# Kernel tuning notes

Measured on AMD Instinct MI355X. Metric: run time of the kernel, lower is better.

Reference implementation:

```python
import jax, jax.numpy as jnp
import numpy as np

D_MODEL = 1024
NUM_HEADS = 16
D_K = D_MODEL // NUM_HEADS


def setup_inputs() -> dict:
    key = jax.random.key(0)
    ks = jax.random.split(key, 11)
    B, S = 2, 2048
    s = 1.0 / np.sqrt(D_MODEL)
    return {
        "query": jax.random.normal(ks[0], (B, S, D_MODEL), jnp.float32),
        "key": jax.random.normal(ks[1], (B, S, D_MODEL), jnp.float32),
        "value": jax.random.normal(ks[2], (B, S, D_MODEL), jnp.float32),
        "Wq": jax.random.normal(ks[3], (D_MODEL, D_MODEL), jnp.float32) * s,
        "bq": jnp.zeros((D_MODEL,), jnp.float32),
        "Wk": jax.random.normal(ks[4], (D_MODEL, D_MODEL), jnp.float32) * s,
        "bk": jnp.zeros((D_MODEL,), jnp.float32),
        "Wv": jax.random.normal(ks[5], (D_MODEL, D_MODEL), jnp.float32) * s,
        "bv": jnp.zeros((D_MODEL,), jnp.float32),
        "Wo": jax.random.normal(ks[6], (D_MODEL, D_MODEL), jnp.float32) * s,
        "bo": jnp.zeros((D_MODEL,), jnp.float32),
    }


def _split_heads(x):
    # [B, S, D] -> [B, H, S, d_k]
    B, S, _ = x.shape
    return x.reshape(B, S, NUM_HEADS, D_K).transpose(0, 2, 1, 3)


def reference(query, key, value, Wq, bq, Wk, bk, Wv, bv, Wo, bo):
    B, S, _ = query.shape
    q = _split_heads(query @ Wq + bq)   # [B, H, S, d_k]
    k = _split_heads(key @ Wk + bk)
    v = _split_heads(value @ Wv + bv)
    scores = jnp.einsum("bhqd,bhkd->bhqk", q, k) / jnp.sqrt(jnp.float32(D_K))
    attention_weights = jax.nn.softmax(scores, axis=-1)  # [B, H, S, S]
    context = jnp.einsum("bhqk,bhkd->bhqd", attention_weights, v)
    context = context.transpose(0, 2, 1, 3).reshape(B, S, D_MODEL)
    output = context @ Wo + bo
    return (output, attention_weights)
```

## Files before the change

### kernel.cpp

```cpp
#include <hip/hip_runtime.h>
#include <hip/hip_bf16.h>


#define SEQ   2048
#define DMODEL 1024
#define NH    16
#define DKH   64

typedef __attribute__((ext_vector_type(8))) short  short8;
typedef __attribute__((ext_vector_type(4))) float  floatx4;

__device__ __forceinline__ short f2bf(float f) {
    __hip_bfloat16 h = __float2bfloat16(f);
    return *reinterpret_cast<short*>(&h);
}

__device__ __forceinline__ void gload_lds16(const short* g, short* l) {
    __builtin_amdgcn_global_load_lds(
        (const __attribute__((address_space(1))) void*)g,
        (__attribute__((address_space(3))) void*)l, 16, 0, 0);
}

__global__ void conv_f32_bf16(const float* __restrict__ src, short* __restrict__ dst, int n4) {
    int i = blockIdx.x * blockDim.x + threadIdx.x;
    if (i < n4) {
        float4 v = reinterpret_cast<const float4*>(src)[i];
        short4 o;
        o.x = f2bf(v.x); o.y = f2bf(v.y); o.z = f2bf(v.z); o.w = f2bf(v.w);
        reinterpret_cast<short4*>(dst)[i] = o;
    }
}

__global__ void conv_wt(const float* __restrict__ W, short* __restrict__ Wt) {
    __shared__ short T[64 * 72];
    int tid = threadIdx.x;
    int bk = blockIdx.y, bn = blockIdx.x;
    for (int i = 0; i < 4; i++) {
        int ch = i * 256 + tid;
        int r = ch >> 4, c4 = (ch & 15) * 4;
        float4 v = *(const float4*)&W[(size_t)(bk * 64 + r) * 1024 + bn * 64 + c4];
        T[(c4 + 0) * 72 + r] = f2bf(v.x);
        T[(c4 + 1) * 72 + r] = f2bf(v.y);
        T[(c4 + 2) * 72 + r] = f2bf(v.z);
        T[(c4 + 3) * 72 + r] = f2bf(v.w);
    }
    __syncthreads();
    for (int i = 0; i < 2; i++) {
        int ch = i * 256 + tid;
        int n = ch >> 3, k8 = (ch & 7) * 8;
        *(short8*)&Wt[(size_t)(bn * 64 + n) * 1024 + bk * 64 + k8] = *(const short8*)&T[n * 72 + k8];
    }
}

__global__ __launch_bounds__(256, 3) void gemm_bf16(
    const short* __restrict__ A, const short* __restrict__ Bt,
    const float* __restrict__ bias, void* __restrict__ dst, int mode)
{
    __shared__ __align__(16) short As[128 * 32];
    __shared__ __align__(16) short Bs[64 * 32];
    int tid = threadIdx.x;
    int wave = tid >> 6, lane = tid & 63, quad = lane >> 4, l15 = lane & 15;
    int bm = blockIdx.y, bn = blockIdx.x;

    floatx4 acc[2][4];
    for (int i = 0; i < 2; i++) for (int j = 0; j < 4; j++) acc[i][j] = (floatx4){0.f, 0.f, 0.f, 0.f};

    for (int kb = 0; kb < 32; kb++) {
        for (int r = 0; r < 2; r++) {
            int ch = r * 256 + tid;
            int row = ch >> 2, kq = (ch & 3) * 8;
            gload_lds16(&A[(size_t)(bm * 128 + row) * 1024 + kb * 32 + kq],
                        &As[(r * 256 + wave * 64) * 8]);
        }
        {
            int row = tid >> 2, kq = (tid & 3) * 8;
            gload_lds16(&Bt[(size_t)(bn * 64 + row) * 1024 + kb * 32 + kq],
                        &Bs[(wave * 64) * 8]);
        }
        __syncthreads();
        short8 ar[2], br[4];
        for (int mt = 0; mt < 2; mt++) ar[mt] = *(const short8*)&As[(wave * 32 + mt * 16 + l15) * 32 + quad * 8];
        for (int nt = 0; nt < 4; nt++) br[nt] = *(const short8*)&Bs[(nt * 16 + l15) * 32 + quad * 8];
        for (int mt = 0; mt < 2; mt++)
            for (int nt = 0; nt < 4; nt++)
                acc[mt][nt] = __builtin_amdgcn_mfma_f32_16x16x32_bf16(ar[mt], br[nt], acc[mt][nt], 0, 0, 0);
        __syncthreads();
    }

    for (int mt = 0; mt < 2; mt++) {
        for (int nt = 0; nt < 4; nt++) {
            int col = bn * 64 + nt * 16 + l15;
            float bb = bias[col];
            for (int r = 0; r < 4; r++) {
                int row = bm * 128 + wave * 32 + mt * 16 + quad * 4 + r;
                float v = acc[mt][nt][r] + bb;
                if (mode == 3) {
                    ((float*)dst)[(size_t)row * 1024 + col] = v;
                } else {
                    int b = row >> 11, s = row & 2047, h = col >> 6, dk = col & 63;
                    size_t idx;
                    if (mode == 0) idx = ((size_t)(b * NH + h) * SEQ + s) * DKH + dk;
                    else           idx = ((size_t)(b * NH + h) * DKH + dk) * SEQ + s;
                    ((short*)dst)[idx] = f2bf(v);
                }
            }
        }
    }
}

__global__ __launch_bounds__(256, 2) void attn(
    const short* __restrict__ Q,
    const short* __restrict__ K,
    const short* __restrict__ Vt,
    float* __restrict__ wout,
    short* __restrict__ ctx)
{
    __shared__ __align__(16) short Qs [64 * 72];
    __shared__ __align__(16) short Ks [128 * 72];
    __shared__ __align__(16) short Vts[64 * 136];
    __shared__ __align__(16) short Ps [64 * 136];
    __shared__ float partial[4][64];
    __shared__ float rinv[64];

    int tid = threadIdx.x, wave = tid >> 6, lane = tid & 63, quad = lane >> 4, l15 = lane & 15;
    int qt = blockIdx.x, bh = blockIdx.y;
    int b = bh >> 4, h = bh & 15;
    const short* qb  = Q  + ((size_t)bh * SEQ + qt * 64) * DKH;
    const short* kbp = K  + (size_t)bh * SEQ * DKH;
    const short* vtb = Vt + (size_t)bh * DKH * SEQ;

    for (int c = 0; c < 2; c++) {
        int ch = tid * 2 + c; int row = ch >> 3, d = (ch & 7) * 8;
        *(short8*)&Qs[row * 72 + d] = *(const short8*)&qb[row * 64 + d];
    }

    float rs[4][4];
    for (int i = 0; i < 4; i++) for (int r = 0; r < 4; r++) rs[i][r] = 0.f;
    floatx4 cacc[4];
    for (int i = 0; i < 4; i++) cacc[i] = (floatx4){0.f, 0.f, 0.f, 0.f};
    int nbase = wave * 32;

    for (int kb = 0; kb < SEQ / 128; kb++) {
        __syncthreads();
        for (int c = 0; c < 4; c++) {
            int ch = tid * 4 + c; int row = ch >> 3, d = (ch & 7) * 8;
            *(short8*)&Ks[row * 72 + d] = *(const short8*)&kbp[(size_t)(kb * 128 + row) * 64 + d];
        }
        for (int c = 0; c < 4; c++) {
            int ch = tid * 4 + c; int dd = ch >> 4, kq = (ch & 15) * 8;
            *(short8*)&Vts[dd * 136 + kq] = *(const short8*)&vtb[(size_t)dd * SEQ + kb * 128 + kq];
        }
        __syncthreads();

        floatx4 sacc[4][2];
        for (int mt = 0; mt < 4; mt++) for (int nt = 0; nt < 2; nt++) sacc[mt][nt] = (floatx4){0.f, 0.f, 0.f, 0.f};
        for (int kt = 0; kt < 2; kt++) {
            short8 ar[4], br[2];
            for (int mt = 0; mt < 4; mt++) ar[mt] = *(const short8*)&Qs[(mt * 16 + l15) * 72 + kt * 32 + quad * 8];
            for (int nt = 0; nt < 2; nt++) br[nt] = *(const short8*)&Ks[(nbase + nt * 16 + l15) * 72 + kt * 32 + quad * 8];
            for (int mt = 0; mt < 4; mt++)
                for (int nt = 0; nt < 2; nt++)
                    sacc[mt][nt] = __builtin_amdgcn_mfma_f32_16x16x32_bf16(ar[mt], br[nt], sacc[mt][nt], 0, 0, 0);
        }
        for (int mt = 0; mt < 4; mt++) {
            for (int r = 0; r < 4; r++) {
                float e0 = __expf(sacc[mt][0][r] * 0.125f);
                float e1 = __expf(sacc[mt][1][r] * 0.125f);
                int row = mt * 16 + quad * 4 + r;
                Ps[row * 136 + nbase + l15]      = f2bf(e0);
                Ps[row * 136 + nbase + 16 + l15] = f2bf(e1);
                rs[mt][r] += e0 + e1;
            }
        }
        __syncthreads();
        for (int kt = 0; kt < 4; kt++) {
            short8 pa = *(const short8*)&Ps[(wave * 16 + l15) * 136 + kt * 32 + quad * 8];
            for (int nt = 0; nt < 4; nt++) {
                short8 vb = *(const short8*)&Vts[(nt * 16 + l15) * 136 + kt * 32 + quad * 8];
                cacc[nt] = __builtin_amdgcn_mfma_f32_16x16x32_bf16(pa, vb, cacc[nt], 0, 0, 0);
            }
        }
    }

    for (int mt = 0; mt < 4; mt++) {
        for (int r = 0; r < 4; r++) {
            float s = rs[mt][r];
            s += __shfl_xor(s, 1, 64); s += __shfl_xor(s, 2, 64);
            s += __shfl_xor(s, 4, 64); s += __shfl_xor(s, 8, 64);
            if (l15 == 0) partial[wave][mt * 16 + quad * 4 + r] = s;
        }
    }
    __syncthreads();
    if (tid < 64) rinv[tid] = 1.f / (partial[0][tid] + partial[1][tid] + partial[2][tid] + partial[3][tid]);
    __syncthreads();

    for (int nt = 0; nt < 4; nt++) {
        for (int r = 0; r < 4; r++) {
            int row = wave * 16 + quad * 4 + r;
            int qg = qt * 64 + row;
            float v = cacc[nt][r] * rinv[row];
            ctx[((size_t)(b * SEQ + qg)) * DMODEL + h * DKH + nt * 16 + l15] = f2bf(v);
        }
    }

    float* wb = wout + ((size_t)bh * SEQ + qt * 64) * SEQ;
    for (int kb = 0; kb < SEQ / 128; kb++) {
        __syncthreads();
        for (int c = 0; c < 4; c++) {
            int ch = tid * 4 + c; int row = ch >> 3, d = (ch & 7) * 8;
            *(short8*)&Ks[row * 72 + d] = *(const short8*)&kbp[(size_t)(kb * 128 + row) * 64 + d];
        }
        __syncthreads();
        floatx4 sacc[4][2];
        for (int mt = 0; mt < 4; mt++) for (int nt = 0; nt < 2; nt++) sacc[mt][nt] = (floatx4){0.f, 0.f, 0.f, 0.f};
        for (int kt = 0; kt < 2; kt++) {
            short8 ar[4], br[2];
            for (int mt = 0; mt < 4; mt++) ar[mt] = *(const short8*)&Qs[(mt * 16 + l15) * 72 + kt * 32 + quad * 8];
            for (int nt = 0; nt < 2; nt++) br[nt] = *(const short8*)&Ks[(nbase + 2 * l15 + nt) * 72 + kt * 32 + quad * 8];
            for (int mt = 0; mt < 4; mt++)
                for (int nt = 0; nt < 2; nt++)
                    sacc[mt][nt] = __builtin_amdgcn_mfma_f32_16x16x32_bf16(ar[mt], br[nt], sacc[mt][nt], 0, 0, 0);
        }
        for (int mt = 0; mt < 4; mt++) {
            for (int r = 0; r < 4; r++) {
                int row = mt * 16 + quad * 4 + r;
                float ri = rinv[row];
                float2 w2;
                w2.x = __expf(sacc[mt][0][r] * 0.125f) * ri;
                w2.y = __expf(sacc[mt][1][r] * 0.125f) * ri;
                *(float2*)&wb[(size_t)row * SEQ + kb * 128 + nbase + 2 * l15] = w2;
            }
        }
    }
}

extern "C" void kernel_launch(void* const* d_in, const int* in_sizes, int n_in,
                              void* d_out, int out_size, void* d_ws, size_t ws_size,
                              hipStream_t stream) {
    const float* query = (const float*)d_in[0];
    const float* key_  = (const float*)d_in[1];
    const float* value = (const float*)d_in[2];
    const float* Wq = (const float*)d_in[3];  const float* bq = (const float*)d_in[4];
    const float* Wk = (const float*)d_in[5];  const float* bk = (const float*)d_in[6];
    const float* Wv = (const float*)d_in[7];  const float* bv = (const float*)d_in[8];
    const float* Wo = (const float*)d_in[9];  const float* bo = (const float*)d_in[10];

    char* ws = (char*)d_ws;
    const size_t MB = 1ull << 20;
    short* xq  = (short*)(ws +  0 * MB);
    short* xk  = (short*)(ws +  8 * MB);
    short* xv  = (short*)(ws + 16 * MB);
    short* wtq = (short*)(ws + 24 * MB);
    short* wtk = (short*)(ws + 26 * MB);
    short* wtv = (short*)(ws + 28 * MB);
    short* wto = (short*)(ws + 30 * MB);
    short* qh  = (short*)(ws + 32 * MB);
    short* kh  = (short*)(ws + 40 * MB);
    short* vth = (short*)(ws + 48 * MB);
    short* ctx = (short*)(ws + 56 * MB);

    float* out0 = (float*)d_out;
    float* wout = out0 + (size_t)4194304;

    conv_f32_bf16<<<4096, 256, 0, stream>>>(query, xq, 1048576);
    conv_f32_bf16<<<4096, 256, 0, stream>>>(key_,  xk, 1048576);
    conv_f32_bf16<<<4096, 256, 0, stream>>>(value, xv, 1048576);
    conv_wt<<<dim3(16, 16), 256, 0, stream>>>(Wq, wtq);
    conv_wt<<<dim3(16, 16), 256, 0, stream>>>(Wk, wtk);
    conv_wt<<<dim3(16, 16), 256, 0, stream>>>(Wv, wtv);
    conv_wt<<<dim3(16, 16), 256, 0, stream>>>(Wo, wto);

    dim3 gg(16, 32);
    gemm_bf16<<<gg, 256, 0, stream>>>(xq, wtq, bq, qh,  0);
    gemm_bf16<<<gg, 256, 0, stream>>>(xk, wtk, bk, kh,  0);
    gemm_bf16<<<gg, 256, 0, stream>>>(xv, wtv, bv, vth, 2);

    attn<<<dim3(SEQ / 64, 32), 256, 0, stream>>>(qh, kh, vth, wout, ctx);

    gemm_bf16<<<gg, 256, 0, stream>>>(ctx, wto, bo, out0, 3);
}
```

Measured before the change: 790.8 us.

## Batch launches, double-buffer GEMM, prefetch K/V, split attention into two kernels

Merges the three input conversions, four weight transposes and three QKV GEMMs into single launches using blockIdx.z. Double-buffers the GEMM LDS tiles so the next K-slice load overlaps the MFMAs, and prefetches K/V tiles into registers in attention. Splits attention into a context pass and a separate weight-writing pass with higher occupancy, passing row inverse sums through workspace. It also packs P stores into 32-bit writes. The cost is extra LDS per block and recomputing Q·K in a second kernel, as before.

```diff
diff --git a/kernel.cpp b/kernel.cpp
--- a/kernel.cpp
+++ b/kernel.cpp
@@ -14,6 +14,9 @@
     __hip_bfloat16 h = __float2bfloat16(f);
     return *reinterpret_cast<short*>(&h);
 }
+__device__ __forceinline__ unsigned int packbf(float a, float b) {
+    return (unsigned int)(unsigned short)f2bf(a) | ((unsigned int)(unsigned short)f2bf(b) << 16);
+}
 
 __device__ __forceinline__ void gload_lds16(const short* g, short* l) {
     __builtin_amdgcn_global_load_lds(
@@ -21,18 +24,27 @@
         (__attribute__((address_space(3))) void*)l, 16, 0, 0);
 }
 
-__global__ void conv_f32_bf16(const float* __restrict__ src, short* __restrict__ dst, int n4) {
+__global__ void conv3(const float* __restrict__ s0, const float* __restrict__ s1,
+                      const float* __restrict__ s2, short* __restrict__ d0,
+                      short* __restrict__ d1, short* __restrict__ d2) {
+    int z = blockIdx.z;
+    const float* src = z == 0 ? s0 : z == 1 ? s1 : s2;
+    short* dst       = z == 0 ? d0 : z == 1 ? d1 : d2;
     int i = blockIdx.x * blockDim.x + threadIdx.x;
-    if (i < n4) {
-        float4 v = reinterpret_cast<const float4*>(src)[i];
-        short4 o;
-        o.x = f2bf(v.x); o.y = f2bf(v.y); o.z = f2bf(v.z); o.w = f2bf(v.w);
-        reinterpret_cast<short4*>(dst)[i] = o;
-    }
-}
-
-__global__ void conv_wt(const float* __restrict__ W, short* __restrict__ Wt) {
+    float4 v = reinterpret_cast<const float4*>(src)[i];
+    short4 o;
+    o.x = f2bf(v.x); o.y = f2bf(v.y); o.z = f2bf(v.z); o.w = f2bf(v.w);
+    reinterpret_cast<short4*>(dst)[i] = o;
+}
+
+__global__ void conv_wt4(const float* __restrict__ W0, const float* __restrict__ W1,
+                         const float* __restrict__ W2, const float* __restrict__ W3,
+                         short* __restrict__ T0, short* __restrict__ T1,
+                         short* __restrict__ T2, short* __restrict__ T3) {
     __shared__ short T[64 * 72];
+    int z = blockIdx.z;
+    const float* W = z == 0 ? W0 : z == 1 ? W1 : z == 2 ? W2 : W3;
+    short* Wt      = z == 0 ? T0 : z == 1 ? T1 : z == 2 ? T2 : T3;
     int tid = threadIdx.x;
     int bk = blockIdx.y, bn = blockIdx.x;
     for (int i = 0; i < 4; i++) {
@@ -52,45 +64,58 @@
     }
 }
 
-__global__ __launch_bounds__(256, 3) void gemm_bf16(
+__device__ __forceinline__ void gemm_body(
     const short* __restrict__ A, const short* __restrict__ Bt,
     const float* __restrict__ bias, void* __restrict__ dst, int mode)
 {
-    __shared__ __align__(16) short As[128 * 32];
-    __shared__ __align__(16) short Bs[64 * 32];
+    __shared__ __align__(16) short As[2][128 * 32];
+    __shared__ __align__(16) short Bs[2][64 * 32];
     int tid = threadIdx.x;
     int wave = tid >> 6, lane = tid & 63, quad = lane >> 4, l15 = lane & 15;
     int bm = blockIdx.y, bn = blockIdx.x;
 
     floatx4 acc[2][4];
-    for (int i = 0; i < 2; i++) for (int j = 0; j < 4; j++) acc[i][j] = (floatx4){0.f, 0.f, 0.f, 0.f};
-
+#pragma unroll
+    for (int i = 0; i < 2; i++)
+#pragma unroll
+        for (int j = 0; j < 4; j++) acc[i][j] = (floatx4){0.f, 0.f, 0.f, 0.f};
+
+    const short* aBase = &A [(size_t)(bm * 128 + (tid >> 2)) * 1024 + (tid & 3) * 8];
+    const short* bBase = &Bt[(size_t)(bn * 64  + (tid >> 2)) * 1024 + (tid & 3) * 8];
+
+#define STAGE(buf, kb) do {                                              \
+        gload_lds16(aBase + (kb) * 32,             &As[buf][(wave * 64) * 8]);         \
+        gload_lds16(aBase + 64 * 1024 + (kb) * 32, &As[buf][(256 + wave * 64) * 8]);   \
+        gload_lds16(bBase + (kb) * 32,             &Bs[buf][(wave * 64) * 8]);         \
+    } while (0)
+
+    STAGE(0, 0);
+    __syncthreads();
+    int cur = 0;
     for (int kb = 0; kb < 32; kb++) {
-        for (int r = 0; r < 2; r++) {
-            int ch = r * 256 + tid;
-            int row = ch >> 2, kq = (ch & 3) * 8;
-            gload_lds16(&A[(size_t)(bm * 128 + row) * 1024 + kb * 32 + kq],
-                        &As[(r * 256 + wave * 64) * 8]);
-        }
-        {
-            int row = tid >> 2, kq = (tid & 3) * 8;
-            gload_lds16(&Bt[(size_t)(bn * 64 + row) * 1024 + kb * 32 + kq],
-                        &Bs[(wave * 64) * 8]);
-        }
-        __syncthreads();
+        if (kb < 31) STAGE(cur ^ 1, kb + 1);
         short8 ar[2], br[4];
-        for (int mt = 0; mt < 2; mt++) ar[mt] = *(const short8*)&As[(wave * 32 + mt * 16 + l15) * 32 + quad * 8];
-        for (int nt = 0; nt < 4; nt++) br[nt] = *(const short8*)&Bs[(nt * 16 + l15) * 32 + quad * 8];
+#pragma unroll
+        for (int mt = 0; mt < 2; mt++) ar[mt] = *(const short8*)&As[cur][(wave * 32 + mt * 16 + l15) * 32 + quad * 8];
+#pragma unroll
+        for (int nt = 0; nt < 4; nt++) br[nt] = *(const short8*)&Bs[cur][(nt * 16 + l15) * 32 + quad * 8];
+#pragma unroll
         for (int mt = 0; mt < 2; mt++)
+#pragma unroll
             for (int nt = 0; nt < 4; nt++)
                 acc[mt][nt] = __builtin_amdgcn_mfma_f32_16x16x32_bf16(ar[mt], br[nt], acc[mt][nt], 0, 0, 0);
         __syncthreads();
-    }
-
+        cur ^= 1;
+    }
+#undef STAGE
+
+#pragma unroll
     for (int mt = 0; mt < 2; mt++) {
+#pragma unroll
         for (int nt = 0; nt < 4; nt++) {
             int col = bn * 64 + nt * 16 + l15;
             float bb = bias[col];
+#pragma unroll
             for (int r = 0; r < 4; r++) {
                 int row = bm * 128 + wave * 32 + mt * 16 + quad * 4 + r;
                 float v = acc[mt][nt][r] + bb;
@@ -108,11 +133,32 @@
     }
 }
 
-__global__ __launch_bounds__(256, 2) void attn(
+__global__ __launch_bounds__(256, 4) void gemm_qkv(
+    const short* __restrict__ xq, const short* __restrict__ xk, const short* __restrict__ xv,
+    const short* __restrict__ wq, const short* __restrict__ wk, const short* __restrict__ wv,
+    const float* __restrict__ bq, const float* __restrict__ bk, const float* __restrict__ bv,
+    short* __restrict__ qh, short* __restrict__ kh, short* __restrict__ vth)
+{
+    int z = blockIdx.z;
+    const short* A  = z == 0 ? xq : z == 1 ? xk : xv;
+    const short* Bt = z == 0 ? wq : z == 1 ? wk : wv;
+    const float* bi = z == 0 ? bq : z == 1 ? bk : bv;
+    short* dst      = z == 0 ? qh : z == 1 ? kh : vth;
+    gemm_body(A, Bt, bi, dst, z == 2 ? 2 : 0);
+}
+
+__global__ __launch_bounds__(256, 4) void gemm_fin(
+    const short* __restrict__ A, const short* __restrict__ Bt,
+    const float* __restrict__ bias, float* __restrict__ dst)
+{
+    gemm_body(A, Bt, bias, dst, 3);
+}
+
+__global__ __launch_bounds__(256, 2) void attn_p1(
     const short* __restrict__ Q,
     const short* __restrict__ K,
     const short* __restrict__ Vt,
-    float* __restrict__ wout,
+    float* __restrict__ rws,
     short* __restrict__ ctx)
 {
     __shared__ __align__(16) short Qs [64 * 72];
@@ -129,60 +175,94 @@
     const short* kbp = K  + (size_t)bh * SEQ * DKH;
     const short* vtb = Vt + (size_t)bh * DKH * SEQ;
 
+#pragma unroll
     for (int c = 0; c < 2; c++) {
         int ch = tid * 2 + c; int row = ch >> 3, d = (ch & 7) * 8;
         *(short8*)&Qs[row * 72 + d] = *(const short8*)&qb[row * 64 + d];
     }
 
+    short8 kreg[4], vreg[4];
+#define LOADKV(kb) do {                                                              \
+        _Pragma("unroll")                                                            \
+        for (int c = 0; c < 4; c++) { int ch = tid * 4 + c; int row = ch >> 3, d = (ch & 7) * 8; \
+            kreg[c] = *(const short8*)&kbp[(size_t)((kb) * 128 + row) * 64 + d]; }   \
+        _Pragma("unroll")                                                            \
+        for (int c = 0; c < 4; c++) { int ch = tid * 4 + c; int dd = ch >> 4, kq = (ch & 15) * 8; \
+            vreg[c] = *(const short8*)&vtb[(size_t)dd * SEQ + (kb) * 128 + kq]; }    \
+    } while (0)
+
+    LOADKV(0);
+
     float rs[4][4];
-    for (int i = 0; i < 4; i++) for (int r = 0; r < 4; r++) rs[i][r] = 0.f;
+#pragma unroll
+    for (int i = 0; i < 4; i++)
+#pragma unroll
+        for (int r = 0; r < 4; r++) rs[i][r] = 0.f;
     floatx4 cacc[4];
+#pragma unroll
     for (int i = 0; i < 4; i++) cacc[i] = (floatx4){0.f, 0.f, 0.f, 0.f};
     int nbase = wave * 32;
 
     for (int kb = 0; kb < SEQ / 128; kb++) {
         __syncthreads();
+#pragma unroll
         for (int c = 0; c < 4; c++) {
             int ch = tid * 4 + c; int row = ch >> 3, d = (ch & 7) * 8;
-            *(short8*)&Ks[row * 72 + d] = *(const short8*)&kbp[(size_t)(kb * 128 + row) * 64 + d];
-        }
+            *(short8*)&Ks[row * 72 + d] = kreg[c];
+        }
+#pragma unroll
         for (int c = 0; c < 4; c++) {
             int ch = tid * 4 + c; int dd = ch >> 4, kq = (ch & 15) * 8;
-            *(short8*)&Vts[dd * 136 + kq] = *(const short8*)&vtb[(size_t)dd * SEQ + kb * 128 + kq];
-        }
-        __syncthreads();
+            *(short8*)&Vts[dd * 136 + kq] = vreg[c];
+        }
+        __syncthreads();
+        if (kb < SEQ / 128 - 1) LOADKV(kb + 1);
 
         floatx4 sacc[4][2];
-        for (int mt = 0; mt < 4; mt++) for (int nt = 0; nt < 2; nt++) sacc[mt][nt] = (floatx4){0.f, 0.f, 0.f, 0.f};
+#pragma unroll
+        for (int mt = 0; mt < 4; mt++)
+#pragma unroll
+            for (int nt = 0; nt < 2; nt++) sacc[mt][nt] = (floatx4){0.f, 0.f, 0.f, 0.f};
+#pragma unroll
         for (int kt = 0; kt < 2; kt++) {
             short8 ar[4], br[2];
+#pragma unroll
             for (int mt = 0; mt < 4; mt++) ar[mt] = *(const short8*)&Qs[(mt * 16 + l15) * 72 + kt * 32 + quad * 8];
-            for (int nt = 0; nt < 2; nt++) br[nt] = *(const short8*)&Ks[(nbase + nt * 16 + l15) * 72 + kt * 32 + quad * 8];
+#pragma unroll
+            for (int nt = 0; nt < 2; nt++) br[nt] = *(const short8*)&Ks[(nbase + 2 * l15 + nt) * 72 + kt * 32 + quad * 8];
+#pragma unroll
             for (int mt = 0; mt < 4; mt++)
+#pragma unroll
                 for (int nt = 0; nt < 2; nt++)
                     sacc[mt][nt] = __builtin_amdgcn_mfma_f32_16x16x32_bf16(ar[mt], br[nt], sacc[mt][nt], 0, 0, 0);
         }
+#pragma unroll
         for (int mt = 0; mt < 4; mt++) {
+#pragma unroll
             for (int r = 0; r < 4; r++) {
                 float e0 = __expf(sacc[mt][0][r] * 0.125f);
                 float e1 = __expf(sacc[mt][1][r] * 0.125f);
                 int row = mt * 16 + quad * 4 + r;
-                Ps[row * 136 + nbase + l15]      = f2bf(e0);
-                Ps[row * 136 + nbase + 16 + l15] = f2bf(e1);
+                *(unsigned int*)&Ps[row * 136 + nbase + 2 * l15] = packbf(e0, e1);
                 rs[mt][r] += e0 + e1;
             }
         }
         __syncthreads();
+#pragma unroll
         for (int kt = 0; kt < 4; kt++) {
             short8 pa = *(const short8*)&Ps[(wave * 16 + l15) * 136 + kt * 32 + quad * 8];
+#pragma unroll
             for (int nt = 0; nt < 4; nt++) {
                 short8 vb = *(const short8*)&Vts[(nt * 16 + l15) * 136 + kt * 32 + quad * 8];
                 cacc[nt] = __builtin_amdgcn_mfma_f32_16x16x32_bf16(pa, vb, cacc[nt], 0, 0, 0);
             }
         }
     }
-
+#undef LOADKV
+
+#pragma unroll
     for (int mt = 0; mt < 4; mt++) {
+#pragma unroll
         for (int r = 0; r < 4; r++) {
             float s = rs[mt][r];
             s += __shfl_xor(s, 1, 64); s += __shfl_xor(s, 2, 64);
@@ -191,10 +271,16 @@
         }
     }
     __syncthreads();
-    if (tid < 64) rinv[tid] = 1.f / (partial[0][tid] + partial[1][tid] + partial[2][tid] + partial[3][tid]);
+    if (tid < 64) {
+        float ri = 1.f / (partial[0][tid] + partial[1][tid] + partial[2][tid] + partial[3][tid]);
+        rinv[tid] = ri;
+        rws[((size_t)bh * 32 + qt) * 64 + tid] = ri;
+    }
     __syncthreads();
 
+#pragma unroll
     for (int nt = 0; nt < 4; nt++) {
+#pragma unroll
         for (int r = 0; r < 4; r++) {
             int row = wave * 16 + quad * 4 + r;
             int qg = qt * 64 + row;
@@ -202,26 +288,70 @@
             ctx[((size_t)(b * SEQ + qg)) * DMODEL + h * DKH + nt * 16 + l15] = f2bf(v);
         }
     }
-
+}
+
+__global__ __launch_bounds__(256, 4) void attn_p2(
+    const short* __restrict__ Q, const short* __restrict__ K,
+    const float* __restrict__ rws, float* __restrict__ wout)
+{
+    __shared__ __align__(16) short Qs[64 * 72];
+    __shared__ __align__(16) short Ks[128 * 72];
+    __shared__ float rinv[64];
+
+    int tid = threadIdx.x, wave = tid >> 6, lane = tid & 63, quad = lane >> 4, l15 = lane & 15;
+    int qt = blockIdx.x, bh = blockIdx.y;
+    const short* qb  = Q + ((size_t)bh * SEQ + qt * 64) * DKH;
+    const short* kbp = K + (size_t)bh * SEQ * DKH;
+
+#pragma unroll
+    for (int c = 0; c < 2; c++) {
+        int ch = tid * 2 + c; int row = ch >> 3, d = (ch & 7) * 8;
+        *(short8*)&Qs[row * 72 + d] = *(const short8*)&qb[row * 64 + d];
+    }
+    if (tid < 64) rinv[tid] = rws[((size_t)bh * 32 + qt) * 64 + tid];
+
+    short8 kreg[4];
+#define LOADK(kb) do {                                                               \
+        _Pragma("unroll")                                                            \
+        for (int c = 0; c < 4; c++) { int ch = tid * 4 + c; int row = ch >> 3, d = (ch & 7) * 8; \
+            kreg[c] = *(const short8*)&kbp[(size_t)((kb) * 128 + row) * 64 + d]; }   \
+    } while (0)
+
+    LOADK(0);
+    int nbase = wave * 32;
     float* wb = wout + ((size_t)bh * SEQ + qt * 64) * SEQ;
+
     for (int kb = 0; kb < SEQ / 128; kb++) {
         __syncthreads();
+#pragma unroll
         for (int c = 0; c < 4; c++) {
             int ch = tid * 4 + c; int row = ch >> 3, d = (ch & 7) * 8;
-            *(short8*)&Ks[row * 72 + d] = *(const short8*)&kbp[(size_t)(kb * 128 + row) * 64 + d];
-        }
-        __syncthreads();
+            *(short8*)&Ks[row * 72 + d] = kreg[c];
+        }
+        __syncthreads();
+        if (kb < SEQ / 128 - 1) LOADK(kb + 1);
+
         floatx4 sacc[4][2];
-        for (int mt = 0; mt < 4; mt++) for (int nt = 0; nt < 2; nt++) sacc[mt][nt] = (floatx4){0.f, 0.f, 0.f, 0.f};
+#pragma unroll
+        for (int mt = 0; mt < 4; mt++)
+#pragma unroll
+            for (int nt = 0; nt < 2; nt++) sacc[mt][nt] = (floatx4){0.f, 0.f, 0.f, 0.f};
+#pragma unroll
         for (int kt = 0; kt < 2; kt++) {
             short8 ar[4], br[2];
+#pragma unroll
             for (int mt = 0; mt < 4; mt++) ar[mt] = *(const short8*)&Qs[(mt * 16 + l15) * 72 + kt * 32 + quad * 8];
+#pragma unroll
             for (int nt = 0; nt < 2; nt++) br[nt] = *(const short8*)&Ks[(nbase + 2 * l15 + nt) * 72 + kt * 32 + quad * 8];
+#pragma unroll
             for (int mt = 0; mt < 4; mt++)
+#pragma unroll
                 for (int nt = 0; nt < 2; nt++)
                     sacc[mt][nt] = __builtin_amdgcn_mfma_f32_16x16x32_bf16(ar[mt], br[nt], sacc[mt][nt], 0, 0, 0);
         }
+#pragma unroll
         for (int mt = 0; mt < 4; mt++) {
+#pragma unroll
             for (int r = 0; r < 4; r++) {
                 int row = mt * 16 + quad * 4 + r;
                 float ri = rinv[row];
@@ -232,6 +362,7 @@
             }
         }
     }
+#undef LOADK
 }
 
 extern "C" void kernel_launch(void* const* d_in, const int* in_sizes, int n_in,
@@ -258,24 +389,19 @@
     short* kh  = (short*)(ws + 40 * MB);
     short* vth = (short*)(ws + 48 * MB);
     short* ctx = (short*)(ws + 56 * MB);
+    float* rws = (float*)(ws +  0 * MB);
 
     float* out0 = (float*)d_out;
     float* wout = out0 + (size_t)4194304;
 
-    conv_f32_bf16<<<4096, 256, 0, stream>>>(query, xq, 1048576);
-    conv_f32_bf16<<<4096, 256, 0, stream>>>(key_,  xk, 1048576);
-    conv_f32_bf16<<<4096, 256, 0, stream>>>(value, xv, 1048576);
-    conv_wt<<<dim3(16, 16), 256, 0, stream>>>(Wq, wtq);
-    conv_wt<<<dim3(16, 16), 256, 0, stream>>>(Wk, wtk);
-    conv_wt<<<dim3(16, 16), 256, 0, stream>>>(Wv, wtv);
-    conv_wt<<<dim3(16, 16), 256, 0, stream>>>(Wo, wto);
-
-    dim3 gg(16, 32);
-    gemm_bf16<<<gg, 256, 0, stream>>>(xq, wtq, bq, qh,  0);
-    gemm_bf16<<<gg, 256, 0, stream>>>(xk, wtk, bk, kh,  0);
-    gemm_bf16<<<gg, 256, 0, stream>>>(xv, wtv, bv, vth, 2);
-
-    attn<<<dim3(SEQ / 64, 32), 256, 0, stream>>>(qh, kh, vth, wout, ctx);
-
-    gemm_bf16<<<gg, 256, 0, stream>>>(ctx, wto, bo, out0, 3);
-}
+    conv3<<<dim3(4096, 1, 3), 256, 0, stream>>>(query, key_, value, xq, xk, xv);
+    conv_wt4<<<dim3(16, 16, 4), 256, 0, stream>>>(Wq, Wk, Wv, Wo, wtq, wtk, wtv, wto);
+
+    gemm_qkv<<<dim3(16, 32, 3), 256, 0, stream>>>(xq, xk, xv, wtq, wtk, wtv,
+                                                  bq, bk, bv, qh, kh, vth);
+
+    attn_p1<<<dim3(SEQ / 64, 32), 256, 0, stream>>>(qh, kh, vth, rws, ctx);
+    attn_p2<<<dim3(SEQ / 64, 32), 256, 0, stream>>>(qh, kh, rws, wout);
+
+    gemm_fin<<<dim3(16, 32), 256, 0, stream>>>(ctx, wto, bo, out0);
+}
```

Result: faster. 759.5 us (-4.0%).
